# Kernel tuning notes

Measured on AMD Instinct MI355X. Metric: run time of the kernel, lower is better.

The kernel has to match this reference:

```python
import jax, jax.numpy as jnp
import numpy as np

B, E, V, T, NSTEP = 32, 256, 32000, 2048, 128  # batch, embed_dim, graph_dim, total_length, min_len


def setup_inputs() -> dict:
    key = jax.random.key(0)
    k1, k2, k3, k4 = jax.random.split(key, 4)
    latent = jax.random.normal(k1, (T, E * E), dtype=jnp.float32) * 0.02
    vocab_w = jax.random.normal(k2, (E, V), dtype=jnp.float32) * 0.02
    vocab_b = jnp.zeros((V,), dtype=jnp.float32)
    zi = jax.random.randint(k3, (B,), 0, T)
    y = jax.random.randint(k4, (B, NSTEP), 0, V)
    return {"latent": latent, "vocab_w": vocab_w, "vocab_b": vocab_b, "zi": zi, "y": y}


def _trajectory(z_flat, n_step):
    # z_flat: [B, E*E] -> per-sample transition matrix [B, E, E]
    trans = z_flat.reshape(-1, E, E)
    z0 = trans[:, 0, :]  # seed state = first row, [B, E]

    def step(z, _):
        # torch .std() is unbiased (ddof=1)
        zn = z / (1e-5 + jnp.std(z, axis=-1, keepdims=True, ddof=1)) * 0.113
        emit = jnp.einsum('be,bef->bf', zn, trans)  # [B, E]
        return emit, emit

    _, zs = jax.lax.scan(step, z0, None, length=n_step)  # [n_step, B, E]
    return jnp.transpose(zs, (1, 0, 2))  # [B, n_step, E]


def reference(latent, vocab_w, vocab_b, zi, y):
    z = latent[zi]                      # [B, E*E]
    zs = _trajectory(z, NSTEP)          # [B, n_step, E]
    logits = zs @ vocab_w + vocab_b     # [B, n_step, V]
    logp = jax.nn.log_softmax(logits, axis=-1)
    yp = jnp.take_along_axis(logp, y[..., None], axis=-1)[..., 0]  # [B, n_step]
    return yp
```

## Files before the change

### kernel.cpp

```cpp
#include <hip/hip_runtime.h>
#include <hip/hip_bf16.h>

#define BATCH 32
#define E 256
#define V 32000
#define NSTEP 128
#define M_TOTAL (BATCH * NSTEP)
#define BM 128
#define BN2 64
#define NBT (V / BN2)
#define NGRP 16
#define NPART (2 * NGRP)

typedef __attribute__((ext_vector_type(4))) float f32x4;
typedef __attribute__((ext_vector_type(2))) float f32x2;
typedef __attribute__((ext_vector_type(8))) short s16x8;
typedef __attribute__((ext_vector_type(4))) unsigned int u32x4;

static __device__ __forceinline__ short f2bf(float v) {
    __hip_bfloat16 h = __float2bfloat16(v);
    return *reinterpret_cast<short*>(&h);
}

static __device__ __forceinline__ unsigned char f2fp8(float v) {
    int p = __builtin_amdgcn_cvt_pk_fp8_f32(v, v, 0, false);
    return (unsigned char)(p & 0xff);
}
template<bool HI>
static __device__ __forceinline__ f32x2 fp8x2_to_f32(unsigned int x) {
    return __builtin_amdgcn_cvt_pk_f32_fp8((int)x, HI);
}

static __device__ __forceinline__ void gload_lds16(const void* g, void* l) {
    __builtin_amdgcn_global_load_lds((const __attribute__((address_space(1))) void*)g,
                                     (__attribute__((address_space(3))) void*)l,
                                     16, 0, 0);
}

template<int CTRL>
static __device__ __forceinline__ float dpp_add(float v) {
    int i = __builtin_amdgcn_update_dpp(0, __builtin_bit_cast(int, v), CTRL, 0xF, 0xF, false);
    return v + __builtin_bit_cast(float, i);
}
static __device__ __forceinline__ float row16_sum(float v) {
    v = dpp_add<0x121>(v);
    v = dpp_add<0x122>(v);
    v = dpp_add<0x124>(v);
    v = dpp_add<0x128>(v);
    return v;
}

__global__ __launch_bounds__(512, 2) void traj_transpose_kernel(
        const float* __restrict__ latent, const int* __restrict__ zi,
        const float* __restrict__ w,
        unsigned char* __restrict__ zsb8, unsigned char* __restrict__ wt8) {
    __shared__ float tile[64][65];
    __shared__ __align__(16) short zsh[E];
    __shared__ __align__(16) float red[16];

    const int tid = threadIdx.x;

    if (blockIdx.x >= BATCH) {
        const int bb = blockIdx.x - BATCH;
        const int k0 = (bb & 3) * 64;
        const int n0 = (bb >> 2) * 64;
        const int c  = tid & 63;
        const int r8 = tid >> 6;
        #pragma unroll
        for (int r = r8; r < 64; r += 8)
            tile[r][c] = w[(size_t)(k0 + r) * V + n0 + c];
        __syncthreads();
        #pragma unroll
        for (int r = r8; r < 64; r += 8)
            wt8[(size_t)(n0 + r) * E + k0 + c] = f2fp8(tile[c][r]);
        return;
    }

    const int b    = blockIdx.x;
    const int lane = tid & 63;
    const int wv   = tid >> 6;
    const int lm   = lane & 15;
    const int g    = lane >> 4;
    const float* tr = latent + (size_t)zi[b] * (E * E);

    s16x8 bfrag[2][8];
    #pragma unroll
    for (int nt = 0; nt < 2; ++nt)
        #pragma unroll
        for (int kk = 0; kk < 8; ++kk) {
            s16x8 fr;
            #pragma unroll
            for (int j = 0; j < 8; ++j)
                fr[j] = f2bf(tr[(size_t)(kk * 32 + g * 8 + j) * E + wv * 32 + nt * 16 + lm]);
            bfrag[nt][kk] = fr;
        }

    if (tid < E) zsh[tid] = f2bf(tr[tid]);

    {
        float v = (tid < E) ? tr[tid] : 0.f;
        float a = row16_sum(v), a2 = row16_sum(v * v);
        a  += __shfl_xor(a, 16);  a2 += __shfl_xor(a2, 16);
        a  += __shfl_xor(a, 32);  a2 += __shfl_xor(a2, 32);
        if (lane == 0) { red[wv] = a; red[8 + wv] = a2; }
    }
    __syncthreads();

    float scale;
    {
        f32x4 p0 = *(const f32x4*)&red[0], p1 = *(const f32x4*)&red[4];
        f32x4 q0 = *(const f32x4*)&red[8], q1 = *(const f32x4*)&red[12];
        float ts  = (p0[0]+p0[1]+p0[2]+p0[3]) + (p1[0]+p1[1]+p1[2]+p1[3]);
        float ts2 = (q0[0]+q0[1]+q0[2]+q0[3]) + (q1[0]+q1[1]+q1[2]+q1[3]);
        float var = fmaxf((ts2 - ts * ts * (1.0f / 256.0f)) * (1.0f / 255.0f), 0.f);
        scale = 0.113f / (1e-5f + sqrtf(var));
    }
    __syncthreads();

    for (int t = 0; t < NSTEP; ++t) {
        s16x8 a[8];
        #pragma unroll
        for (int kk = 0; kk < 8; ++kk)
            a[kk] = *(const s16x8*)((const char*)zsh + kk * 64 + g * 16);

        f32x4 acc0 = {}, acc1 = {};
        #pragma unroll
        for (int kk = 0; kk < 8; ++kk) {
            acc0 = __builtin_amdgcn_mfma_f32_16x16x32_bf16(a[kk], bfrag[0][kk], acc0, 0, 0, 0);
            acc1 = __builtin_amdgcn_mfma_f32_16x16x32_bf16(a[kk], bfrag[1][kk], acc1, 0, 0, 0);
        }

        float u  = row16_sum(acc0[0] + acc1[0]);
        float u2 = row16_sum(acc0[0] * acc0[0] + acc1[0] * acc1[0]);
        if (lane == 0) { red[wv] = u; red[8 + wv] = u2; }
        __syncthreads();

        f32x4 p0 = *(const f32x4*)&red[0], p1 = *(const f32x4*)&red[4];
        f32x4 q0 = *(const f32x4*)&red[8], q1 = *(const f32x4*)&red[12];
        float ts  = (p0[0]+p0[1]+p0[2]+p0[3]) + (p1[0]+p1[1]+p1[2]+p1[3]);
        float ts2 = (q0[0]+q0[1]+q0[2]+q0[3]) + (q1[0]+q1[1]+q1[2]+q1[3]);
        float var = fmaxf((ts2 - ts * ts * (1.0f / 256.0f)) * (1.0f / 255.0f), 0.f);
        float stdr = sqrtf(var);

        float e0 = scale * acc0[0], e1 = scale * acc1[0];
        if (g == 0) {
            zsh[wv * 32 + lm]      = f2bf(e0);
            zsh[wv * 32 + 16 + lm] = f2bf(e1);
            unsigned char* zr = zsb8 + ((size_t)b * NSTEP + t) * E + wv * 32;
            zr[lm]      = f2fp8(e0);
            zr[16 + lm] = f2fp8(e1);
        }
        scale = 0.113f / (1e-5f + scale * stdr);
        __syncthreads();
    }
}

__global__ __launch_bounds__(256, 2) void gemm_lse_kernel(const unsigned char* __restrict__ zsb8,
                                                          const unsigned char* __restrict__ wt8,
                                                          const float* __restrict__ vb,
                                                          float* __restrict__ partial) {
    __shared__ unsigned char apan[BM * E];
    __shared__ unsigned char bpan[2][BN2 * E];

    const int tid  = threadIdx.x;
    const int lane = tid & 63;
    const int w    = tid >> 6;
    const int bm   = blockIdx.x >> 4;
    const int grp  = blockIdx.x & 15;
    const int m0   = bm * BM;
    const int t0   = (NBT * grp) >> 4;
    const int t1   = (NBT * (grp + 1)) >> 4;

    #pragma unroll
    for (int i = 0; i < 8; ++i) {
        const int c   = i * 256 + tid;
        const int row = c >> 4;
        const int gsl = ((c & 15) - row) & 15;
        gload_lds16(zsb8 + (size_t)(m0 + row) * E + gsl * 16, (char*)apan + c * 16);
    }
    {
        const int n0 = t0 * BN2;
        #pragma unroll
        for (int i = 0; i < 4; ++i) {
            const int c   = i * 256 + tid;
            const int row = c >> 4;
            const int gsl = ((c & 15) - row) & 15;
            gload_lds16(wt8 + (size_t)(n0 + row) * E + gsl * 16, (char*)bpan[0] + c * 16);
        }
    }

    const int wr = w >> 1, wc = w & 1;
    const int lm = lane & 15, lk = lane >> 4;
    const int h  = (lk & 1) * 8;

    float rs[4][4] = {};

    __syncthreads();

    for (int i = t0; i < t1; ++i) {
        const int cur = (i - t0) & 1;
        if (i + 1 < t1) {
            const int n0n = (i + 1) * BN2;
            #pragma unroll
            for (int j = 0; j < 4; ++j) {
                const int c   = j * 256 + tid;
                const int row = c >> 4;
                const int gsl = ((c & 15) - row) & 15;
                gload_lds16(wt8 + (size_t)(n0n + row) * E + gsl * 16,
                            (char*)bpan[cur ^ 1] + c * 16);
            }
        }

        const int n0 = i * BN2;
        const float bias0 = vb[n0 + wc * 32 + lm];
        const float bias1 = vb[n0 + wc * 32 + 16 + lm];

        f32x4 acc[4][2] = {};
        const unsigned char* bp = bpan[cur];
        #pragma unroll
        for (int kk = 0; kk < 8; ++kk) {
            const int c0 = kk * 2 + (lk >> 1);
            long long bfr[2];
            #pragma unroll
            for (int nt = 0; nt < 2; ++nt) {
                const int rn = wc * 32 + nt * 16 + lm;
                bfr[nt] = *(const long long*)(bp + rn * 256 + ((c0 + rn) & 15) * 16 + h);
            }
            #pragma unroll
            for (int rt = 0; rt < 4; ++rt) {
                const int ra = wr * 64 + rt * 16 + lm;
                const long long af = *(const long long*)(apan + ra * 256 + ((c0 + ra) & 15) * 16 + h);
                acc[rt][0] = __builtin_amdgcn_mfma_f32_16x16x32_fp8_fp8(af, bfr[0], acc[rt][0], 0, 0, 0);
                acc[rt][1] = __builtin_amdgcn_mfma_f32_16x16x32_fp8_fp8(af, bfr[1], acc[rt][1], 0, 0, 0);
            }
        }

        #pragma unroll
        for (int rt = 0; rt < 4; ++rt)
            #pragma unroll
            for (int r = 0; r < 4; ++r)
                rs[rt][r] += __expf(acc[rt][0][r] + bias0) + __expf(acc[rt][1][r] + bias1);

        __syncthreads();
    }

    const int cr = lane >> 4;
    #pragma unroll
    for (int rt = 0; rt < 4; ++rt)
        #pragma unroll
        for (int r = 0; r < 4; ++r) {
            const float v = row16_sum(rs[rt][r]);
            if (lm == 0)
                partial[(size_t)(grp * 2 + wc) * M_TOTAL + m0 + wr * 64 + rt * 16 + cr * 4 + r] = v;
        }
}

__global__ __launch_bounds__(256) void finalize_kernel(const unsigned char* __restrict__ zsb8,
                                                       const unsigned char* __restrict__ wt8,
                                                       const float* __restrict__ vb,
                                                       const int* __restrict__ y,
                                                       const float* __restrict__ partial,
                                                       float* __restrict__ out) {
    const int tid  = threadIdx.x;
    const int lane = tid & 63;
    const int rw   = lane >> 4;
    const int kl   = lane & 15;
    const int row  = blockIdx.x * 16 + (tid >> 6) * 4 + rw;
    const int yrow = y[row];

    u32x4 za = *(const u32x4*)(zsb8 + (size_t)row * E + kl * 16);
    u32x4 wa = *(const u32x4*)(wt8 + (size_t)yrow * E + kl * 16);
    float acc = 0.f;
    #pragma unroll
    for (int q = 0; q < 4; ++q) {
        f32x2 a0 = fp8x2_to_f32<false>(za[q]), b0 = fp8x2_to_f32<false>(wa[q]);
        f32x2 a1 = fp8x2_to_f32<true>(za[q]),  b1 = fp8x2_to_f32<true>(wa[q]);
        acc += a0[0] * b0[0] + a0[1] * b0[1] + a1[0] * b1[0] + a1[1] * b1[1];
    }
    const float logit = row16_sum(acc) + vb[yrow];

    float ps = partial[(size_t)kl * M_TOTAL + row] + partial[(size_t)(kl + 16) * M_TOTAL + row];
    const float tot = row16_sum(ps);

    if (kl == 0) out[row] = logit - logf(tot);
}

extern "C" void kernel_launch(void* const* d_in, const int* in_sizes, int n_in,
                              void* d_out, int out_size, void* d_ws, size_t ws_size,
                              hipStream_t stream) {
    const float* latent  = (const float*)d_in[0];
    const float* vocab_w = (const float*)d_in[1];
    const float* vocab_b = (const float*)d_in[2];
    const int*   zi      = (const int*)d_in[3];
    const int*   y       = (const int*)d_in[4];
    float* out = (float*)d_out;

    char* ws = (char*)d_ws;
    float*         partial = (float*)(ws);
    unsigned char* zsb8    = (unsigned char*)(ws + 524288);
    unsigned char* wt8     = (unsigned char*)(ws + 524288 + 1048576);

    hipLaunchKernelGGL(traj_transpose_kernel, dim3(BATCH + 4 * (V / 64)), dim3(512), 0, stream,
                       latent, zi, vocab_w, zsb8, wt8);
    hipLaunchKernelGGL(gemm_lse_kernel, dim3(32 * NGRP), dim3(256), 0, stream,
                       zsb8, wt8, vocab_b, partial);
    hipLaunchKernelGGL(finalize_kernel, dim3(M_TOTAL / 16), dim3(256), 0, stream,
                       zsb8, wt8, vocab_b, y, partial, out);
}
```

Measured before the change: 160.4 us.

## Permute K layout for register-resident A, widen N tile, double-buffer trajectory

```diff
diff --git a/kernel.cpp b/kernel.cpp
--- a/kernel.cpp
+++ b/kernel.cpp
@@ -7,7 +7,7 @@
 #define NSTEP 128
 #define M_TOTAL (BATCH * NSTEP)
 #define BM 128
-#define BN2 64
+#define BN2 128
 #define NBT (V / BN2)
 #define NGRP 16
 #define NPART (2 * NGRP)
@@ -29,6 +29,14 @@
 template<bool HI>
 static __device__ __forceinline__ f32x2 fp8x2_to_f32(unsigned int x) {
     return __builtin_amdgcn_cvt_pk_f32_fp8((int)x, HI);
+}
+
+static __device__ __forceinline__ int fragpos(int e) {
+    return ((e >> 3) & 3) * 64 + (e >> 5) * 8 + (e & 7);
+}
+
+static __device__ __forceinline__ long long ll2(unsigned int a, unsigned int b) {
+    return (long long)(((unsigned long long)b << 32) | a);
 }
 
 static __device__ __forceinline__ void gload_lds16(const void* g, void* l) {
@@ -55,8 +63,8 @@
         const float* __restrict__ w,
         unsigned char* __restrict__ zsb8, unsigned char* __restrict__ wt8) {
     __shared__ float tile[64][65];
-    __shared__ __align__(16) short zsh[E];
-    __shared__ __align__(16) float red[16];
+    __shared__ __align__(16) short zsh[2][E];
+    __shared__ __align__(16) float red[2][16];
 
     const int tid = threadIdx.x;
 
@@ -70,9 +78,10 @@
         for (int r = r8; r < 64; r += 8)
             tile[r][c] = w[(size_t)(k0 + r) * V + n0 + c];
         __syncthreads();
+        const int fp = fragpos(k0 + c);
         #pragma unroll
         for (int r = r8; r < 64; r += 8)
-            wt8[(size_t)(n0 + r) * E + k0 + c] = f2fp8(tile[c][r]);
+            wt8[(size_t)(n0 + r) * E + fp] = f2fp8(tile[c][r]);
         return;
     }
 
@@ -95,33 +104,36 @@
             bfrag[nt][kk] = fr;
         }
 
-    if (tid < E) zsh[tid] = f2bf(tr[tid]);
+    if (tid < E) zsh[0][tid] = f2bf(tr[tid]);
 
     {
         float v = (tid < E) ? tr[tid] : 0.f;
         float a = row16_sum(v), a2 = row16_sum(v * v);
         a  += __shfl_xor(a, 16);  a2 += __shfl_xor(a2, 16);
         a  += __shfl_xor(a, 32);  a2 += __shfl_xor(a2, 32);
-        if (lane == 0) { red[wv] = a; red[8 + wv] = a2; }
+        if (lane == 0) { red[1][wv] = a; red[1][8 + wv] = a2; }
     }
     __syncthreads();
 
     float scale;
     {
-        f32x4 p0 = *(const f32x4*)&red[0], p1 = *(const f32x4*)&red[4];
-        f32x4 q0 = *(const f32x4*)&red[8], q1 = *(const f32x4*)&red[12];
+        f32x4 p0 = *(const f32x4*)&red[1][0], p1 = *(const f32x4*)&red[1][4];
+        f32x4 q0 = *(const f32x4*)&red[1][8], q1 = *(const f32x4*)&red[1][12];
         float ts  = (p0[0]+p0[1]+p0[2]+p0[3]) + (p1[0]+p1[1]+p1[2]+p1[3]);
         float ts2 = (q0[0]+q0[1]+q0[2]+q0[3]) + (q1[0]+q1[1]+q1[2]+q1[3]);
         float var = fmaxf((ts2 - ts * ts * (1.0f / 256.0f)) * (1.0f / 255.0f), 0.f);
         scale = 0.113f / (1e-5f + sqrtf(var));
     }
-    __syncthreads();
+
+    const int p0i = fragpos(wv * 32 + lm);
+    const int p1i = fragpos(wv * 32 + 16 + lm);
 
     for (int t = 0; t < NSTEP; ++t) {
+        const short* zrd = zsh[t & 1];
         s16x8 a[8];
         #pragma unroll
         for (int kk = 0; kk < 8; ++kk)
-            a[kk] = *(const s16x8*)((const char*)zsh + kk * 64 + g * 16);
+            a[kk] = *(const s16x8*)((const char*)zrd + kk * 64 + g * 16);
 
         f32x4 acc0 = {}, acc1 = {};
         #pragma unroll
@@ -130,28 +142,27 @@
             acc1 = __builtin_amdgcn_mfma_f32_16x16x32_bf16(a[kk], bfrag[1][kk], acc1, 0, 0, 0);
         }
 
+        const float e0 = scale * acc0[0], e1 = scale * acc1[0];
+        if (g == 0) {
+            zsh[(t + 1) & 1][wv * 32 + lm]      = f2bf(e0);
+            zsh[(t + 1) & 1][wv * 32 + 16 + lm] = f2bf(e1);
+            unsigned char* zr = zsb8 + ((size_t)b * NSTEP + t) * E;
+            zr[p0i] = f2fp8(e0);
+            zr[p1i] = f2fp8(e1);
+        }
+
         float u  = row16_sum(acc0[0] + acc1[0]);
         float u2 = row16_sum(acc0[0] * acc0[0] + acc1[0] * acc1[0]);
-        if (lane == 0) { red[wv] = u; red[8 + wv] = u2; }
+        if (lane == 0) { red[t & 1][wv] = u; red[t & 1][8 + wv] = u2; }
         __syncthreads();
 
-        f32x4 p0 = *(const f32x4*)&red[0], p1 = *(const f32x4*)&red[4];
-        f32x4 q0 = *(const f32x4*)&red[8], q1 = *(const f32x4*)&red[12];
-        float ts  = (p0[0]+p0[1]+p0[2]+p0[3]) + (p1[0]+p1[1]+p1[2]+p1[3]);
-        float ts2 = (q0[0]+q0[1]+q0[2]+q0[3]) + (q1[0]+q1[1]+q1[2]+q1[3]);
+        const float* rd = red[t & 1];
+        f32x4 r0 = *(const f32x4*)&rd[0], r1 = *(const f32x4*)&rd[4];
+        f32x4 s0 = *(const f32x4*)&rd[8], s1 = *(const f32x4*)&rd[12];
+        float ts  = (r0[0]+r0[1]+r0[2]+r0[3]) + (r1[0]+r1[1]+r1[2]+r1[3]);
+        float ts2 = (s0[0]+s0[1]+s0[2]+s0[3]) + (s1[0]+s1[1]+s1[2]+s1[3]);
         float var = fmaxf((ts2 - ts * ts * (1.0f / 256.0f)) * (1.0f / 255.0f), 0.f);
-        float stdr = sqrtf(var);
-
-        float e0 = scale * acc0[0], e1 = scale * acc1[0];
-        if (g == 0) {
-            zsh[wv * 32 + lm]      = f2bf(e0);
-            zsh[wv * 32 + 16 + lm] = f2bf(e1);
-            unsigned char* zr = zsb8 + ((size_t)b * NSTEP + t) * E + wv * 32;
-            zr[lm]      = f2fp8(e0);
-            zr[16 + lm] = f2fp8(e1);
-        }
-        scale = 0.113f / (1e-5f + scale * stdr);
-        __syncthreads();
+        scale = 0.113f / (1e-5f + scale * sqrtf(var));
     }
 }
 
@@ -159,7 +170,6 @@
                                                           const unsigned char* __restrict__ wt8,
                                                           const float* __restrict__ vb,
                                                           float* __restrict__ partial) {
-    __shared__ unsigned char apan[BM * E];
     __shared__ unsigned char bpan[2][BN2 * E];
 
     const int tid  = threadIdx.x;
@@ -171,27 +181,30 @@
     const int t0   = (NBT * grp) >> 4;
     const int t1   = (NBT * (grp + 1)) >> 4;
 
+    const int wr = w >> 1, wc = w & 1;
+    const int lm = lane & 15, lk = lane >> 4;
+    const int mw = m0 + wr * 64;
+
+    long long areg[4][8];
     #pragma unroll
-    for (int i = 0; i < 8; ++i) {
-        const int c   = i * 256 + tid;
-        const int row = c >> 4;
-        const int gsl = ((c & 15) - row) & 15;
-        gload_lds16(zsb8 + (size_t)(m0 + row) * E + gsl * 16, (char*)apan + c * 16);
-    }
+    for (int rt = 0; rt < 4; ++rt)
+        #pragma unroll
+        for (int kp = 0; kp < 4; ++kp) {
+            u32x4 v = *(const u32x4*)(zsb8 + (size_t)(mw + rt * 16 + lm) * E + lk * 64 + kp * 16);
+            areg[rt][2 * kp]     = ll2(v[0], v[1]);
+            areg[rt][2 * kp + 1] = ll2(v[2], v[3]);
+        }
+
     {
-        const int n0 = t0 * BN2;
-        #pragma unroll
-        for (int i = 0; i < 4; ++i) {
+        const size_t gbase = (size_t)(t0 * BN2) * E;
+        #pragma unroll
+        for (int i = 0; i < 8; ++i) {
             const int c   = i * 256 + tid;
             const int row = c >> 4;
             const int gsl = ((c & 15) - row) & 15;
-            gload_lds16(wt8 + (size_t)(n0 + row) * E + gsl * 16, (char*)bpan[0] + c * 16);
-        }
-    }
-
-    const int wr = w >> 1, wc = w & 1;
-    const int lm = lane & 15, lk = lane >> 4;
-    const int h  = (lk & 1) * 8;
+            gload_lds16(wt8 + gbase + (size_t)row * E + gsl * 16, (char*)bpan[0] + c * 16);
+        }
+    }
 
     float rs[4][4] = {};
 
@@ -200,46 +213,56 @@
     for (int i = t0; i < t1; ++i) {
         const int cur = (i - t0) & 1;
         if (i + 1 < t1) {
-            const int n0n = (i + 1) * BN2;
-            #pragma unroll
-            for (int j = 0; j < 4; ++j) {
+            const size_t gbase = (size_t)((i + 1) * BN2) * E;
+            #pragma unroll
+            for (int j = 0; j < 8; ++j) {
                 const int c   = j * 256 + tid;
                 const int row = c >> 4;
                 const int gsl = ((c & 15) - row) & 15;
-                gload_lds16(wt8 + (size_t)(n0n + row) * E + gsl * 16,
+                gload_lds16(wt8 + gbase + (size_t)row * E + gsl * 16,
                             (char*)bpan[cur ^ 1] + c * 16);
             }
         }
 
         const int n0 = i * BN2;
-        const float bias0 = vb[n0 + wc * 32 + lm];
-        const float bias1 = vb[n0 + wc * 32 + 16 + lm];
-
-        f32x4 acc[4][2] = {};
+        float bias[4];
+        #pragma unroll
+        for (int nt = 0; nt < 4; ++nt) bias[nt] = vb[n0 + wc * 64 + nt * 16 + lm];
+
+        f32x4 acc[4][4] = {};
         const unsigned char* bp = bpan[cur];
         #pragma unroll
-        for (int kk = 0; kk < 8; ++kk) {
-            const int c0 = kk * 2 + (lk >> 1);
-            long long bfr[2];
-            #pragma unroll
-            for (int nt = 0; nt < 2; ++nt) {
-                const int rn = wc * 32 + nt * 16 + lm;
-                bfr[nt] = *(const long long*)(bp + rn * 256 + ((c0 + rn) & 15) * 16 + h);
+        for (int kp = 0; kp < 4; ++kp) {
+            long long blo[4], bhi[4];
+            #pragma unroll
+            for (int nt = 0; nt < 4; ++nt) {
+                const int rn   = wc * 64 + nt * 16 + lm;
+                const int slot = (lk * 4 + kp + rn) & 15;
+                u32x4 bv = *(const u32x4*)(bp + rn * 256 + slot * 16);
+                blo[nt] = ll2(bv[0], bv[1]);
+                bhi[nt] = ll2(bv[2], bv[3]);
             }
             #pragma unroll
-            for (int rt = 0; rt < 4; ++rt) {
-                const int ra = wr * 64 + rt * 16 + lm;
-                const long long af = *(const long long*)(apan + ra * 256 + ((c0 + ra) & 15) * 16 + h);
-                acc[rt][0] = __builtin_amdgcn_mfma_f32_16x16x32_fp8_fp8(af, bfr[0], acc[rt][0], 0, 0, 0);
-                acc[rt][1] = __builtin_amdgcn_mfma_f32_16x16x32_fp8_fp8(af, bfr[1], acc[rt][1], 0, 0, 0);
-            }
+            for (int rt = 0; rt < 4; ++rt)
+                #pragma unroll
+                for (int nt = 0; nt < 4; ++nt)
+                    acc[rt][nt] = __builtin_amdgcn_mfma_f32_16x16x32_fp8_fp8(
+                        areg[rt][2 * kp], blo[nt], acc[rt][nt], 0, 0, 0);
+            #pragma unroll
+            for (int rt = 0; rt < 4; ++rt)
+                #pragma unroll
+                for (int nt = 0; nt < 4; ++nt)
+                    acc[rt][nt] = __builtin_amdgcn_mfma_f32_16x16x32_fp8_fp8(
+                        areg[rt][2 * kp + 1], bhi[nt], acc[rt][nt], 0, 0, 0);
         }
 
         #pragma unroll
         for (int rt = 0; rt < 4; ++rt)
             #pragma unroll
-            for (int r = 0; r < 4; ++r)
-                rs[rt][r] += __expf(acc[rt][0][r] + bias0) + __expf(acc[rt][1][r] + bias1);
+            for (int nt = 0; nt < 4; ++nt)
+                #pragma unroll
+                for (int r = 0; r < 4; ++r)
+                    rs[rt][r] += __expf(acc[rt][nt][r] + bias[nt]);
 
         __syncthreads();
     }
@@ -251,7 +274,7 @@
         for (int r = 0; r < 4; ++r) {
             const float v = row16_sum(rs[rt][r]);
             if (lm == 0)
-                partial[(size_t)(grp * 2 + wc) * M_TOTAL + m0 + wr * 64 + rt * 16 + cr * 4 + r] = v;
+                partial[(size_t)(grp * 2 + wc) * M_TOTAL + mw + rt * 16 + cr * 4 + r] = v;
         }
 }
 
```

Result: faster. 152.8 us (-4.7%).
